# Optimization experiments

Hardware: AMD Instinct MI355X
Metric: run time of the kernel (lower is better)

The kernel has to match this reference:

```python
import jax, jax.numpy as jnp
import numpy as np

KERNEL_MUL = 2.0
KERNEL_NUM = 5

N_S = 4096
N_T = 4096
D = 512
N_CLS = 10


def setup_inputs() -> dict:
    key = jax.random.key(0)
    k1, k2, k3 = jax.random.split(key, 3)
    x = jax.random.normal(k1, (N_S + N_T, D), dtype=jnp.float32)
    # source-first domain labels: first N_S are source (0), rest target (1)
    domain_labels = jnp.concatenate(
        [jnp.zeros((N_S,), dtype=jnp.int32), jnp.ones((N_T,), dtype=jnp.int32)]
    )
    y_true = jax.random.randint(k2, (N_S,), 0, N_CLS, dtype=jnp.int32)
    im_weights = jax.random.uniform(k3, (N_CLS,), dtype=jnp.float32, minval=0.5, maxval=1.5)
    return {
        "x": x,
        "im_weights": im_weights,
        "domain_labels": domain_labels,
        "y_true": y_true,
        "alpha": 1,
    }


def _gaussian_kernel_sum(total, n_samples):
    # Pairwise squared L2 distances via Gram trick instead of the O(N^2*D)
    # broadcasted tensor the torch code materializes (same math).
    sq = jnp.sum(total * total, axis=1)                      # [N]
    l2 = sq[:, None] + sq[None, :] - 2.0 * (total @ total.T)  # [N, N]
    l2 = jnp.maximum(l2, 0.0)
    # bandwidth computed on detached distances (torch uses L2_distance.data)
    bandwidth = jnp.sum(jax.lax.stop_gradient(l2)) / float(n_samples * n_samples - n_samples)
    bandwidth = bandwidth / (KERNEL_MUL ** (KERNEL_NUM // 2))
    k = jnp.zeros_like(l2)
    for i in range(KERNEL_NUM):
        k = k + jnp.exp(-l2 / (bandwidth * (KERNEL_MUL ** i)))
    return k


def reference(x, im_weights, domain_labels, y_true, alpha):
    dl = np.asarray(domain_labels)  # int labels are concrete constants
    src = np.where(dl == 0)[0]
    tgt = np.where(dl == 1)[0]
    n_s, n_t = len(src), len(tgt)

    total = jnp.concatenate([x[src], x[tgt]], axis=0)        # [n_s+n_t, D]
    kernels = _gaussian_kernel_sum(total, n_s + n_t)         # [N, N]

    # importance weights are detached in the torch code
    iw = jax.lax.stop_gradient(alpha * im_weights + (1.0 - alpha))
    w = iw[y_true]                                           # [n_s]

    k_ss = kernels[:n_s, :n_s]
    k_tt = kernels[n_s:, n_s:]
    k_st = kernels[:n_s, n_s:]

    # loss_1: weighted source upper-triangle + unweighted target upper-triangle
    loss_1 = jnp.sum(jnp.triu(k_ss * (w[:, None] * w[None, :]), k=1)) / float(n_s * (n_s - 1) / 2)
    loss_1 = loss_1 + jnp.sum(jnp.triu(k_tt, k=1)) / float(n_t * (n_t - 1) / 2)

    # loss_2: cross term, weighted by source sample weights
    loss_2 = jnp.sum(k_st * w[:, None]) / float(n_s * n_t)

    return loss_1 - 2.0 * loss_2
```

## Files before the change

### kernel.cpp

```cpp
#include <hip/hip_runtime.h>
#include <math.h>

#define N_TOT 8192
#define N_SRC 4096
#define D_DIM 512
#define BM 128
#define NT (N_TOT / BM)
#define NTILES (NT * (NT + 1) / 2)
#define NPREP 256

typedef short bf16x8 __attribute__((ext_vector_type(8)));
typedef unsigned short u16x8 __attribute__((ext_vector_type(8)));
typedef float f32x4 __attribute__((ext_vector_type(4)));


__device__ __forceinline__ unsigned short f2bf_rn(float v) {
    unsigned int u = __float_as_uint(v);
    unsigned int r = (u + 0x7FFFu + ((u >> 16) & 1u)) >> 16;
    return (unsigned short)r;
}

__global__ __launch_bounds__(256) void k_prep(const float* __restrict__ x,
                                              unsigned short* __restrict__ xhi,
                                              unsigned short* __restrict__ xlo,
                                              float* __restrict__ sq,
                                              float* __restrict__ colpart) {
    const int wave = threadIdx.x >> 6;
    const int lane = threadIdx.x & 63;
    __shared__ float colbuf[4][512];
    float fcol[8];
#pragma unroll
    for (int j = 0; j < 8; ++j) fcol[j] = 0.f;

#pragma unroll
    for (int r8 = 0; r8 < 8; ++r8) {
        const int row = blockIdx.x * 32 + wave * 8 + r8;
        const size_t base = (size_t)row * D_DIM + lane * 8;
        float v[8];
        *(float4*)&v[0] = *(const float4*)(x + base);
        *(float4*)&v[4] = *(const float4*)(x + base + 4);
        u16x8 h, l;
        float s = 0.f;
#pragma unroll
        for (int j = 0; j < 8; ++j) {
            unsigned short hb = f2bf_rn(v[j]);
            float hv = __uint_as_float(((unsigned int)hb) << 16);
            h[j] = hb;
            l[j] = f2bf_rn(v[j] - hv);
            s = fmaf(v[j], v[j], s);
            fcol[j] += v[j];
        }
        *(u16x8*)(xhi + base) = h;
        *(u16x8*)(xlo + base) = l;
#pragma unroll
        for (int off = 32; off; off >>= 1) s += __shfl_xor(s, off);
        if (lane == 0) sq[row] = s;
    }
#pragma unroll
    for (int j = 0; j < 8; ++j) colbuf[wave][lane * 8 + j] = fcol[j];
    __syncthreads();
    const int c = threadIdx.x * 2;
    float2 r;
    r.x = colbuf[0][c] + colbuf[1][c] + colbuf[2][c] + colbuf[3][c];
    r.y = colbuf[0][c + 1] + colbuf[1][c + 1] + colbuf[2][c + 1] + colbuf[3][c + 1];
    *(float2*)(colpart + (size_t)blockIdx.x * D_DIM + c) = r;
}

__global__ __launch_bounds__(256) void k_bw(const float* __restrict__ sq,
                                            const float* __restrict__ colpart,
                                            const float* __restrict__ imw,
                                            const int* __restrict__ y,
                                            const int* __restrict__ alpha_p,
                                            float* __restrict__ w,
                                            float* __restrict__ invbw,
                                            double* __restrict__ accum,
                                            unsigned int* __restrict__ cnt) {
    const int tid = threadIdx.x;
    if (tid == 0) { accum[2] = 0.0; *cnt = 0u; }
    const float a = (float)alpha_p[0];
    for (int i = tid; i < N_SRC; i += 256) w[i] = a * imw[y[i]] + (1.0f - a);
    double s2 = 0.0;
    for (int i = tid; i < N_TOT; i += 256) s2 += (double)sq[i];
    double cs0 = 0.0, cs1 = 0.0;
    const int c = tid * 2;
#pragma unroll 8
    for (int b = 0; b < NPREP; ++b) {
        float2 v = *(const float2*)(colpart + (size_t)b * D_DIM + c);
        cs0 += (double)v.x;
        cs1 += (double)v.y;
    }
    double sc = cs0 * cs0 + cs1 * cs1;
    __shared__ double r1[256], r2[256];
    r1[tid] = s2; r2[tid] = sc;
    __syncthreads();
    for (int off = 128; off; off >>= 1) {
        if (tid < off) { r1[tid] += r1[tid + off]; r2[tid] += r2[tid + off]; }
        __syncthreads();
    }
    if (tid == 0) {
        double sum_l2 = 2.0 * (double)N_TOT * r1[0] - 2.0 * r2[0];
        double bw = sum_l2 / ((double)N_TOT * (double)N_TOT - (double)N_TOT);
        bw *= 0.25;
        double m = 1.0;
        for (int i = 0; i < 5; ++i) { invbw[i] = (float)(1.0 / (bw * m)); m *= 2.0; }
    }
}

__device__ __forceinline__ void gload_lds16(const unsigned short* g, char* l) {
    __builtin_amdgcn_global_load_lds((const __attribute__((address_space(1))) void*)g,
                                     (__attribute__((address_space(3))) void*)l,
                                     16, 0, 0);
}

__device__ __forceinline__ int swz_of(int row) { return (row & 3) ^ ((row >> 2) & 3); }

__global__ __launch_bounds__(256, 3) void k_pairs(const unsigned short* __restrict__ xhi,
                                                  const unsigned short* __restrict__ xlo,
                                                  const float* __restrict__ sq,
                                                  const float* __restrict__ w,
                                                  const float* __restrict__ invbw,
                                                  double* __restrict__ accum,
                                                  unsigned int* __restrict__ cnt,
                                                  float* __restrict__ out) {
    int bid = (blockIdx.x & 7) * (NTILES / 8) + (blockIdx.x >> 3);
    int ti = 0, rem = bid;
    while (rem >= NT - ti) { rem -= NT - ti; ++ti; }
    const int tj = ti + rem;
    const int i0 = ti * BM, j0 = tj * BM;

    __shared__ __align__(16) char lds[2 * 24576];
    __shared__ double sdl4[4];

    const int tid = threadIdx.x;
    const int lane = tid & 63;
    const int wave = tid >> 6;
    const int wr = wave >> 1, wc = wave & 1;
    const int lr = lane & 15, lg = lane >> 4;

    f32x4 acc[4][4];
#pragma unroll
    for (int m = 0; m < 4; ++m)
#pragma unroll
        for (int n = 0; n < 4; ++n) acc[m][n] = f32x4{0.f, 0.f, 0.f, 0.f};

    const unsigned short* srcs[3] = {xhi + (size_t)i0 * D_DIM, xlo + (size_t)i0 * D_DIM,
                                     xhi + (size_t)j0 * D_DIM};

#define STAGE(P, KK)                                                                   \
    do {                                                                               \
        _Pragma("unroll") for (int t6 = 0; t6 < 6; ++t6) {                             \
            int idx = t6 * 256 + tid;                                                  \
            int tile = idx >> 9;                                                       \
            int ci = idx & 511;                                                        \
            int row = ci >> 2, cc = ci & 3;                                            \
            int cg = cc ^ swz_of(row);                                                 \
            gload_lds16(srcs[tile] + (size_t)row * D_DIM + (KK) + cg * 8,              \
                        lds + (P) * 24576 + idx * 16);                                 \
        }                                                                              \
    } while (0)

    STAGE(0, 0);
    asm volatile("s_waitcnt vmcnt(0)\n\ts_barrier" ::: "memory");
    __builtin_amdgcn_sched_barrier(0);

#pragma unroll
    for (int t = 0; t < 16; ++t) {
        const int cur = t & 1;
        if (t < 15) STAGE(cur ^ 1, (t + 1) * 32);

        const char* lAh = lds + cur * 24576;
        const char* lAl = lAh + 8192;
        const char* lBh = lAh + 16384;
        bf16x8 ah[4], al[4], bh[4];
#pragma unroll
        for (int m = 0; m < 4; ++m) {
            int row = wr * 64 + m * 16 + lr;
            int off = row * 64 + ((lg ^ swz_of(row)) << 4);
            ah[m] = *(const bf16x8*)(lAh + off);
            al[m] = *(const bf16x8*)(lAl + off);
        }
#pragma unroll
        for (int n = 0; n < 4; ++n) {
            int row = wc * 64 + n * 16 + lr;
            int off = row * 64 + ((lg ^ swz_of(row)) << 4);
            bh[n] = *(const bf16x8*)(lBh + off);
        }
        __builtin_amdgcn_s_setprio(1);
#pragma unroll
        for (int m = 0; m < 4; ++m)
#pragma unroll
            for (int n = 0; n < 4; ++n) {
                acc[m][n] = __builtin_amdgcn_mfma_f32_16x16x32_bf16(ah[m], bh[n], acc[m][n], 0, 0, 0);
                acc[m][n] = __builtin_amdgcn_mfma_f32_16x16x32_bf16(al[m], bh[n], acc[m][n], 0, 0, 0);
            }
        __builtin_amdgcn_s_setprio(0);
        asm volatile("s_waitcnt lgkmcnt(0)" ::: "memory");
        __builtin_amdgcn_sched_barrier(0);
        asm volatile("s_waitcnt vmcnt(0)\n\ts_barrier" ::: "memory");
        __builtin_amdgcn_sched_barrier(0);
    }
#undef STAGE

    float sqi[4][4], wi[4][4], sqj[4], wj[4];
#pragma unroll
    for (int m = 0; m < 4; ++m)
#pragma unroll
        for (int j = 0; j < 4; ++j) {
            int i = i0 + wr * 64 + m * 16 + lg * 4 + j;
            sqi[m][j] = sq[i];
            wi[m][j] = (i < N_SRC) ? w[i] : 0.f;
        }
#pragma unroll
    for (int n = 0; n < 4; ++n) {
        int jg = j0 + wc * 64 + n * 16 + lr;
        sqj[n] = sq[jg];
        wj[n] = (jg < N_SRC) ? w[jg] : 0.f;
    }
    const float nib4 = -invbw[4];

    const bool diag = (ti == tj);
    const int region = (tj < NT / 2) ? 0 : ((ti >= NT / 2) ? 1 : 2);

    float facc = 0.f;
#pragma unroll
    for (int m = 0; m < 4; ++m)
#pragma unroll
        for (int n = 0; n < 4; ++n)
#pragma unroll
            for (int j = 0; j < 4; ++j) {
                int rg = wr * 64 + m * 16 + lg * 4 + j;
                int cg = wc * 64 + n * 16 + lr;
                if (diag && rg >= cg) continue;
                float l2 = fmaf(-2.f, acc[m][n][j], sqi[m][j] + sqj[n]);
                l2 = fmaxf(l2, 0.f);
                float t = __expf(l2 * nib4);
                float t2 = t * t, t4 = t2 * t2, t8 = t4 * t4, t16 = t8 * t8;
                float k5 = t + t2 + t4 + t8 + t16;
                float cf;
                if (region == 0)      cf = wi[m][j] * wj[n];
                else if (region == 1) cf = 1.f;
                else                  cf = wi[m][j];
                facc = fmaf(k5, cf, facc);
            }

#pragma unroll
    for (int off = 32; off; off >>= 1) facc += __shfl_xor(facc, off);
    if (lane == 0) sdl4[wave] = (double)facc;
    __syncthreads();
    if (tid == 0) {
        const double C_SS = 1.0 / 8386560.0;
        const double C_ST = 2.0 / 16777216.0;
        double scale = (region == 2) ? -C_ST : C_SS;
        atomicAdd(&accum[2], scale * (sdl4[0] + sdl4[1] + sdl4[2] + sdl4[3]));
        __threadfence();
        unsigned int old = atomicAdd(cnt, 1u);
        if (old == NTILES - 1) {
            double v = atomicAdd(&accum[2], 0.0);
            out[0] = (float)v;
        }
    }
}

extern "C" void kernel_launch(void* const* d_in, const int* in_sizes, int n_in,
                              void* d_out, int out_size, void* d_ws, size_t ws_size,
                              hipStream_t stream) {
    const float* x    = (const float*)d_in[0];
    const float* imw  = (const float*)d_in[1];
    const int*   y    = (const int*)d_in[3];
    const int*   alph = (const int*)d_in[4];
    float* out = (float*)d_out;

    char* ws = (char*)d_ws;
    double*       accum   = (double*)ws;
    unsigned int* cnt     = (unsigned int*)(ws + 64);
    float*        invbw   = (float*)(ws + 128);
    float*        sq      = (float*)(ws + 4096);
    float*        wgt     = (float*)(ws + 36864);
    float*        colpart = (float*)(ws + 53248);
    unsigned short* xhi   = (unsigned short*)(ws + 577536);
    unsigned short* xlo   = (unsigned short*)(ws + 8966144);

    k_prep<<<NPREP, 256, 0, stream>>>(x, xhi, xlo, sq, colpart);
    k_bw<<<1, 256, 0, stream>>>(sq, colpart, imw, y, alph, wgt, invbw, accum, cnt);
    k_pairs<<<NTILES, 256, 0, stream>>>(xhi, xlo, sq, wgt, invbw, accum, cnt, out);
}
```

Measured before the change: 217.7 us.

## Drop bf16 lo-part split in Gram GEMM and triple-buffer LDS staging

Removes the hi/lo bf16 split compensation, so the Gram matrix uses a single bf16 product per pair instead of two. This halves MFMA work and removes one of the three operand tiles from loading and staging. The LDS pipeline also moves from double to triple buffering with partial vmcnt waits, so loads run two stages ahead. The cost is lower precision in the pairwise distances, and the loss may drift from the fp32 reference.

```diff
diff --git a/kernel.cpp b/kernel.cpp
--- a/kernel.cpp
+++ b/kernel.cpp
@@ -22,7 +22,6 @@
 
 __global__ __launch_bounds__(256) void k_prep(const float* __restrict__ x,
                                               unsigned short* __restrict__ xhi,
-                                              unsigned short* __restrict__ xlo,
                                               float* __restrict__ sq,
                                               float* __restrict__ colpart) {
     const int wave = threadIdx.x >> 6;
@@ -39,19 +38,15 @@
         float v[8];
         *(float4*)&v[0] = *(const float4*)(x + base);
         *(float4*)&v[4] = *(const float4*)(x + base + 4);
-        u16x8 h, l;
+        u16x8 h;
         float s = 0.f;
 #pragma unroll
         for (int j = 0; j < 8; ++j) {
-            unsigned short hb = f2bf_rn(v[j]);
-            float hv = __uint_as_float(((unsigned int)hb) << 16);
-            h[j] = hb;
-            l[j] = f2bf_rn(v[j] - hv);
+            h[j] = f2bf_rn(v[j]);
             s = fmaf(v[j], v[j], s);
             fcol[j] += v[j];
         }
         *(u16x8*)(xhi + base) = h;
-        *(u16x8*)(xlo + base) = l;
 #pragma unroll
         for (int off = 32; off; off >>= 1) s += __shfl_xor(s, off);
         if (lane == 0) sq[row] = s;
@@ -115,7 +110,6 @@
 __device__ __forceinline__ int swz_of(int row) { return (row & 3) ^ ((row >> 2) & 3); }
 
 __global__ __launch_bounds__(256, 3) void k_pairs(const unsigned short* __restrict__ xhi,
-                                                  const unsigned short* __restrict__ xlo,
                                                   const float* __restrict__ sq,
                                                   const float* __restrict__ w,
                                                   const float* __restrict__ invbw,
@@ -128,7 +122,7 @@
     const int tj = ti + rem;
     const int i0 = ti * BM, j0 = tj * BM;
 
-    __shared__ __align__(16) char lds[2 * 24576];
+    __shared__ __align__(16) char lds[3 * 16384];
     __shared__ double sdl4[4];
 
     const int tid = threadIdx.x;
@@ -143,41 +137,39 @@
 #pragma unroll
         for (int n = 0; n < 4; ++n) acc[m][n] = f32x4{0.f, 0.f, 0.f, 0.f};
 
-    const unsigned short* srcs[3] = {xhi + (size_t)i0 * D_DIM, xlo + (size_t)i0 * D_DIM,
-                                     xhi + (size_t)j0 * D_DIM};
+    const unsigned short* srcs[2] = {xhi + (size_t)i0 * D_DIM, xhi + (size_t)j0 * D_DIM};
 
 #define STAGE(P, KK)                                                                   \
     do {                                                                               \
-        _Pragma("unroll") for (int t6 = 0; t6 < 6; ++t6) {                             \
-            int idx = t6 * 256 + tid;                                                  \
+        _Pragma("unroll") for (int t4 = 0; t4 < 4; ++t4) {                             \
+            int idx = t4 * 256 + tid;                                                  \
             int tile = idx >> 9;                                                       \
             int ci = idx & 511;                                                        \
             int row = ci >> 2, cc = ci & 3;                                            \
             int cg = cc ^ swz_of(row);                                                 \
             gload_lds16(srcs[tile] + (size_t)row * D_DIM + (KK) + cg * 8,              \
-                        lds + (P) * 24576 + idx * 16);                                 \
+                        lds + (P) * 16384 + idx * 16);                                 \
         }                                                                              \
     } while (0)
 
     STAGE(0, 0);
-    asm volatile("s_waitcnt vmcnt(0)\n\ts_barrier" ::: "memory");
+    STAGE(1, 32);
+    asm volatile("s_waitcnt vmcnt(4)\n\ts_barrier" ::: "memory");
     __builtin_amdgcn_sched_barrier(0);
 
 #pragma unroll
     for (int t = 0; t < 16; ++t) {
-        const int cur = t & 1;
-        if (t < 15) STAGE(cur ^ 1, (t + 1) * 32);
-
-        const char* lAh = lds + cur * 24576;
-        const char* lAl = lAh + 8192;
-        const char* lBh = lAh + 16384;
-        bf16x8 ah[4], al[4], bh[4];
+        const int cur = t % 3;
+        if (t < 14) STAGE((t + 2) % 3, (t + 2) * 32);
+
+        const char* lAh = lds + cur * 16384;
+        const char* lBh = lAh + 8192;
+        bf16x8 ah[4], bh[4];
 #pragma unroll
         for (int m = 0; m < 4; ++m) {
             int row = wr * 64 + m * 16 + lr;
             int off = row * 64 + ((lg ^ swz_of(row)) << 4);
             ah[m] = *(const bf16x8*)(lAh + off);
-            al[m] = *(const bf16x8*)(lAl + off);
         }
 #pragma unroll
         for (int n = 0; n < 4; ++n) {
@@ -189,15 +181,17 @@
 #pragma unroll
         for (int m = 0; m < 4; ++m)
 #pragma unroll
-            for (int n = 0; n < 4; ++n) {
+            for (int n = 0; n < 4; ++n)
                 acc[m][n] = __builtin_amdgcn_mfma_f32_16x16x32_bf16(ah[m], bh[n], acc[m][n], 0, 0, 0);
-                acc[m][n] = __builtin_amdgcn_mfma_f32_16x16x32_bf16(al[m], bh[n], acc[m][n], 0, 0, 0);
-            }
         __builtin_amdgcn_s_setprio(0);
-        asm volatile("s_waitcnt lgkmcnt(0)" ::: "memory");
-        __builtin_amdgcn_sched_barrier(0);
-        asm volatile("s_waitcnt vmcnt(0)\n\ts_barrier" ::: "memory");
-        __builtin_amdgcn_sched_barrier(0);
+
+        if (t < 14) {
+            asm volatile("s_waitcnt lgkmcnt(0) vmcnt(4)\n\ts_barrier" ::: "memory");
+            __builtin_amdgcn_sched_barrier(0);
+        } else if (t == 14) {
+            asm volatile("s_waitcnt lgkmcnt(0) vmcnt(0)\n\ts_barrier" ::: "memory");
+            __builtin_amdgcn_sched_barrier(0);
+        }
     }
 #undef STAGE
 
@@ -278,9 +272,8 @@
     float*        wgt     = (float*)(ws + 36864);
     float*        colpart = (float*)(ws + 53248);
     unsigned short* xhi   = (unsigned short*)(ws + 577536);
-    unsigned short* xlo   = (unsigned short*)(ws + 8966144);
-
-    k_prep<<<NPREP, 256, 0, stream>>>(x, xhi, xlo, sq, colpart);
+
+    k_prep<<<NPREP, 256, 0, stream>>>(x, xhi, sq, colpart);
     k_bw<<<1, 256, 0, stream>>>(sq, colpart, imw, y, alph, wgt, invbw, accum, cnt);
-    k_pairs<<<NTILES, 256, 0, stream>>>(xhi, xlo, sq, wgt, invbw, accum, cnt, out);
-}
+    k_pairs<<<NTILES, 256, 0, stream>>>(xhi, sq, wgt, invbw, accum, cnt, out);
+}
```

New measurement: 188.2 us. 1.16x faster.
